# Performance work log

Measured on AMD Instinct MI355X. Metric: run time of the kernel, lower is better.

The kernel has to match this reference:

```python
import jax, jax.numpy as jnp
import numpy as np

NUM_HEADS = 16
HIDDEN = 1024
B, S = 2, 2048


def setup_inputs() -> dict:
    key = jax.random.key(0)
    ks = jax.random.split(key, 14)
    D = HIDDEN
    scale = 1.0 / np.sqrt(D)
    inp = {
        "query": jax.random.normal(ks[0], (B, S, D), jnp.float32),
        "key_in": jax.random.normal(ks[1], (B, S, D), jnp.float32),
        "value": jax.random.normal(ks[2], (B, S, D), jnp.float32),
        "group_prob": jax.random.uniform(ks[3], (B, S, S), jnp.float32),
        "mask": jax.random.randint(ks[4], (B, S, S), 0, 2, jnp.int32),
        "wq_k": jax.random.normal(ks[5], (D, D), jnp.float32) * scale,
        "wq_b": jnp.zeros((D,), jnp.float32),
        "wk_k": jax.random.normal(ks[6], (D, D), jnp.float32) * scale,
        "wk_b": jnp.zeros((D,), jnp.float32),
        "wv_k": jax.random.normal(ks[7], (D, D), jnp.float32) * scale,
        "wv_b": jnp.zeros((D,), jnp.float32),
        "wo_k": jax.random.normal(ks[8], (D, D), jnp.float32) * scale,
        "wo_b": jnp.zeros((D,), jnp.float32),
    }
    return inp


def _split_heads(x, H):
    b, s, d = x.shape
    return x.reshape(b, s, H, d // H).transpose(0, 2, 1, 3)  # (B,H,S,dh)


def reference(query, key_in, value, group_prob, mask,
              wq_k, wq_b, wk_k, wk_b, wv_k, wv_b, wo_k, wo_b):
    H = NUM_HEADS
    dh = query.shape[-1] // H
    q = _split_heads(query @ wq_k + wq_b, H)
    k = _split_heads(key_in @ wk_k + wk_b, H)
    v = _split_heads(value @ wv_k + wv_b, H)
    # scaled dot-product logits (B,H,Sq,Sk)
    logits = jnp.einsum('bhqd,bhkd->bhqk', q, k) / jnp.sqrt(jnp.asarray(dh, q.dtype))
    neg = (1.0 - mask.astype(q.dtype)) * -1e9
    logits = logits + neg[:, None, :, :]
    attn = jax.nn.softmax(logits, axis=-1)
    # Tree Transformer modulation: post-softmax elementwise scale by group_prob
    attn = attn * group_prob[:, None, :, :]
    out = jnp.einsum('bhqk,bhkd->bhqd', attn, v)
    out = out.transpose(0, 2, 1, 3).reshape(query.shape[0], -1, H * dh)
    return out @ wo_k + wo_b
```

## Files before the change

kernel.cpp:

```cpp
#include <hip/hip_runtime.h>
#include <hip/hip_bf16.h>
#include <stdint.h>

#define B_ 2
#define S_ 2048
#define D_ 1024
#define H_ 16
#define DH 64

typedef __attribute__((ext_vector_type(4))) float f32x4;
typedef __attribute__((ext_vector_type(8))) short s16x8;
typedef __attribute__((ext_vector_type(4))) short s16x4;

__device__ inline short f2bf(float f) {
  union { float f; unsigned u; } v; v.f = f;
  unsigned r = (v.u + 0x7fffu + ((v.u >> 16) & 1u)) >> 16;
  return (short)r;
}

__device__ inline float bfbits_lo(unsigned u) {
  union { unsigned x; float f; } v; v.x = u << 16; return v.f;
}
__device__ inline float bfbits_hi(unsigned u) {
  union { unsigned x; float f; } v; v.x = u & 0xffff0000u; return v.f;
}

__device__ inline float exp2v(float x) {
  float r; asm("v_exp_f32 %0, %1" : "=v"(r) : "v"(x)); return r;
}
__device__ inline unsigned cvtpk(float a, float b) {
  unsigned r; asm("v_cvt_pk_bf16_f32 %0, %1, %2" : "=v"(r) : "v"(a), "v"(b));
  return r;
}

__global__ __launch_bounds__(256) void cvt3_f32_bf16(const float* __restrict__ a,
                                                     const float* __restrict__ b,
                                                     const float* __restrict__ c,
                                                     short* oa, short* ob, short* oc,
                                                     int n) {
  int z = blockIdx.y;
  const float* in = z == 0 ? a : (z == 1 ? b : c);
  short* out = z == 0 ? oa : (z == 1 ? ob : oc);
  int i = (blockIdx.x * 256 + threadIdx.x) * 4;
  if (i < n) {
    float4 v = *(const float4*)(in + i);
    s16x4 o;
    o.x = f2bf(v.x); o.y = f2bf(v.y); o.z = f2bf(v.z); o.w = f2bf(v.w);
    *(s16x4*)(out + i) = o;
  }
}

__global__ __launch_bounds__(256) void fuse_mgp(const int* __restrict__ mask,
                                                const float* __restrict__ gp,
                                                short* __restrict__ mgp, int n) {
  int i = (blockIdx.x * 256 + threadIdx.x) * 4;
  if (i < n) {
    int4 m = *(const int4*)(mask + i);
    float4 g = *(const float4*)(gp + i);
    short b0 = f2bf(g.x); if (!b0) b0 = (short)0x0080;
    short b1 = f2bf(g.y); if (!b1) b1 = (short)0x0080;
    short b2 = f2bf(g.z); if (!b2) b2 = (short)0x0080;
    short b3 = f2bf(g.w); if (!b3) b3 = (short)0x0080;
    s16x4 o;
    o.x = m.x ? b0 : 0;
    o.y = m.y ? b1 : 0;
    o.z = m.z ? b2 : 0;
    o.w = m.w ? b3 : 0;
    *(s16x4*)(mgp + i) = o;
  }
}

__global__ __launch_bounds__(256) void transpose_cvt4(
    const float* __restrict__ i0, const float* __restrict__ i1,
    const float* __restrict__ i2, const float* __restrict__ i3,
    short* o0, short* o1, short* o2, short* o3) {
  int z = blockIdx.z;
  const float* in = z == 0 ? i0 : (z == 1 ? i1 : (z == 2 ? i2 : i3));
  short* out = z == 0 ? o0 : (z == 1 ? o1 : (z == 2 ? o2 : o3));
  __shared__ float tile[32][33];
  int bx = blockIdx.x, by = blockIdx.y;
  int x = bx * 32 + threadIdx.x;
#pragma unroll
  for (int i = 0; i < 32; i += 8) {
    int y = by * 32 + threadIdx.y + i;
    tile[threadIdx.y + i][threadIdx.x] = in[(size_t)y * D_ + x];
  }
  __syncthreads();
  int ox = by * 32 + threadIdx.x;
#pragma unroll
  for (int i = 0; i < 32; i += 8) {
    int oy = bx * 32 + threadIdx.y + i;
    out[(size_t)oy * D_ + ox] = f2bf(tile[threadIdx.x][threadIdx.y + i]);
  }
}

__global__ __launch_bounds__(256) void transpose_v(const short* __restrict__ vp,
                                                   short* __restrict__ vt) {
  __shared__ __align__(16) short t[64 * 72];
  int tid = threadIdx.x;
  int bh = blockIdx.y, b = bh >> 4, h = bh & 15;
  int s0 = blockIdx.x * 64;
  int r = tid >> 2, cc = tid & 3;
  const short* src = vp + ((size_t)(b * S_ + s0 + r)) * D_ + h * DH + cc * 16;
  s16x8 a = *(const s16x8*)src;
  s16x8 bb = *(const s16x8*)(src + 8);
  int pc = (cc ^ (r >> 4)) * 16;
  *(s16x8*)&t[r * 72 + pc] = a;
  *(s16x8*)&t[r * 72 + pc + 8] = bb;
  __syncthreads();
  int d = tid >> 2, sc = (tid & 3) * 16;
  s16x8 o0, o1;
#pragma unroll
  for (int j = 0; j < 8; ++j) {
    int row = sc + j;
    o0[j] = t[row * 72 + ((d >> 4) ^ (row >> 4)) * 16 + (d & 15)];
    int row2 = sc + 8 + j;
    o1[j] = t[row2 * 72 + ((d >> 4) ^ (row2 >> 4)) * 16 + (d & 15)];
  }
  short* dst = vt + ((size_t)(b * H_ + h) * DH + d) * S_ + s0 + sc;
  *(s16x8*)dst = o0;
  *(s16x8*)(dst + 8) = o1;
}

__device__ inline void gload_lds16(const void* g, void* l) {
  __builtin_amdgcn_global_load_lds(
      (const __attribute__((address_space(1))) unsigned*)g,
      (__attribute__((address_space(3))) unsigned*)l, 16, 0, 0);
}

#define BM 128
#define BN 128
#define BK 32

__global__ __launch_bounds__(256) void gemm_bt3(
    const short* __restrict__ A0, const short* __restrict__ A1, const short* __restrict__ A2,
    const short* __restrict__ Bt0, const short* __restrict__ Bt1, const short* __restrict__ Bt2,
    const float* __restrict__ bs0, const float* __restrict__ bs1, const float* __restrict__ bs2,
    void* C0, void* C1, void* C2,
    int M, int N, int K, int f32out, float os0, float os1, float os2) {
  int z = blockIdx.y;
  const short* A = z == 0 ? A0 : (z == 1 ? A1 : A2);
  const short* Bt = z == 0 ? Bt0 : (z == 1 ? Bt1 : Bt2);
  const float* bias = z == 0 ? bs0 : (z == 1 ? bs1 : bs2);
  void* C = z == 0 ? C0 : (z == 1 ? C1 : C2);
  float oscale = z == 0 ? os0 : (z == 1 ? os1 : os2);

  __shared__ __align__(16) short As[BM * BK];
  __shared__ __align__(16) short Bs[BN * BK];
  int tid = threadIdx.x;
  int lane = tid & 63, wave = tid >> 6;
  int l15 = lane & 15, l4 = lane >> 4;
  int ntn = N / BN;
  int bm = blockIdx.x / ntn, bn = blockIdx.x % ntn;
  int row0 = bm * BM, col0 = bn * BN;
  int wm = (wave >> 1) * 64, wn = (wave & 1) * 64;

  f32x4 acc[4][4] = {};

  for (int k0 = 0; k0 < K; k0 += BK) {
    __syncthreads();
#pragma unroll
    for (int it = 0; it < 2; ++it) {
      int ch = it * 256 + tid;
      int r = ch >> 2, c = (ch & 3) * 8;
      int ldsbase = (it * 256 + wave * 64) * 8;
      gload_lds16(A + (size_t)(row0 + r) * K + k0 + c, &As[ldsbase]);
      gload_lds16(Bt + (size_t)(col0 + r) * K + k0 + c, &Bs[ldsbase]);
    }
    __syncthreads();
    s16x8 af[4], bf[4];
#pragma unroll
    for (int mf = 0; mf < 4; ++mf)
      af[mf] = *(const s16x8*)&As[(wm + mf * 16 + l15) * BK + l4 * 8];
#pragma unroll
    for (int nf = 0; nf < 4; ++nf)
      bf[nf] = *(const s16x8*)&Bs[(wn + nf * 16 + l15) * BK + l4 * 8];
#pragma unroll
    for (int mf = 0; mf < 4; ++mf)
#pragma unroll
      for (int nf = 0; nf < 4; ++nf)
        acc[mf][nf] = __builtin_amdgcn_mfma_f32_16x16x32_bf16(af[mf], bf[nf],
                                                              acc[mf][nf], 0, 0, 0);
  }

#pragma unroll
  for (int nf = 0; nf < 4; ++nf) {
    int gcol = col0 + wn + nf * 16 + l15;
    float bv = bias[gcol];
#pragma unroll
    for (int mf = 0; mf < 4; ++mf) {
#pragma unroll
      for (int r = 0; r < 4; ++r) {
        int grow = row0 + wm + mf * 16 + l4 * 4 + r;
        float v = (acc[mf][nf][r] + bv) * oscale;
        if (f32out)
          ((float*)C)[(size_t)grow * N + gcol] = v;
        else
          ((short*)C)[(size_t)grow * N + gcol] = f2bf(v);
      }
    }
  }
}

#define QB 64
#define NB 64
#define NTILES (S_ / NB)
#define M0_SHIFT 12.0f

__global__ __launch_bounds__(256) void attn_fused(const short* __restrict__ Qp,
                                                  const short* __restrict__ Kp,
                                                  const short* __restrict__ VT,
                                                  const short* __restrict__ MGP,
                                                  short* __restrict__ ctx) {
  __shared__ __align__(16) short Ks[2][64 * 64];
  __shared__ __align__(16) short Ms[2][64 * 64];
  __shared__ __align__(16) short Vs[2][64 * 64];

  int tid = threadIdx.x, lane = tid & 63, wave = tid >> 6;
  int l15 = lane & 15, l4 = lane >> 4;
  int q0 = blockIdx.x * QB;
  int bh = blockIdx.y;
  int b = bh >> 4, h = bh & 15;
  int wq = wave * 16;

  const short* Qbase = Qp + (size_t)b * S_ * D_ + (size_t)h * DH;
  const short* Kbase = Kp + (size_t)b * S_ * D_ + (size_t)h * DH;
  const short* Vbase = VT + (size_t)(b * H_ + h) * DH * S_;
  const short* Mbase = MGP + (size_t)b * S_ * S_ + (size_t)q0 * S_;

  int i0 = tid, i1 = 256 + tid;
  int r0 = i0 >> 3, c0 = (i0 & 7) ^ (r0 & 7);
  int r1 = i1 >> 3, c1 = (i1 & 7) ^ (r1 & 7);
  int ldsA = wave * 512;
  int ldsB = 2048 + wave * 512;

#define STAGE(kv0, buf)                                                    \
  do {                                                                     \
    gload_lds16(Kbase + (size_t)((kv0) + r0) * D_ + c0 * 8, &Ks[buf][ldsA]); \
    gload_lds16(Kbase + (size_t)((kv0) + r1) * D_ + c1 * 8, &Ks[buf][ldsB]); \
    gload_lds16(Mbase + (size_t)r0 * S_ + (kv0) + c0 * 8, &Ms[buf][ldsA]);   \
    gload_lds16(Mbase + (size_t)r1 * S_ + (kv0) + c1 * 8, &Ms[buf][ldsB]);   \
    gload_lds16(Vbase + (size_t)r0 * S_ + (kv0) + c0 * 8, &Vs[buf][ldsA]);   \
    gload_lds16(Vbase + (size_t)r1 * S_ + (kv0) + c1 * 8, &Vs[buf][ldsB]);   \
  } while (0)

  s16x8 qf[2];
#pragma unroll
  for (int ks = 0; ks < 2; ++ks)
    qf[ks] = *(const s16x8*)(Qbase + (size_t)(q0 + wq + l15) * D_ + ks * 32 + l4 * 8);

  float lsum = 0.f;
  f32x4 oacc[4] = {};

  STAGE(0, 0);

  int ql = wq + l15;
  int rowoff = ql * 64;
  int q7 = l15 & 7;
  int q7l = q7 << 1;

  for (int t = 0; t < NTILES; ++t) {
    int buf = t & 1;

    if (t + 1 < NTILES) {
      STAGE((t + 1) * NB, buf ^ 1);
      asm volatile("s_waitcnt vmcnt(6)" ::: "memory");
    } else {
      asm volatile("s_waitcnt vmcnt(0)" ::: "memory");
    }
    __builtin_amdgcn_s_barrier();
    __builtin_amdgcn_sched_barrier(0);

    f32x4 sacc[4] = {};
#pragma unroll
    for (int nf = 0; nf < 4; ++nf) {
      int R = nf * 16 + l15;
#pragma unroll
      for (int ks = 0; ks < 2; ++ks) {
        s16x8 kf = *(const s16x8*)&Ks[buf][R * 64 + (((ks * 4 + l4) ^ q7) * 8)];
        sacc[nf] = __builtin_amdgcn_mfma_f32_16x16x32_bf16(kf, qf[ks], sacc[nf], 0, 0, 0);
      }
    }

#pragma unroll
    for (int nf = 0; nf < 4; ++nf) {
      int sl = ((nf * 4 + l4) ^ q7l) * 4;
      uint2 g2 = *(const uint2*)&Ms[buf][rowoff + sl];
      float gv0 = bfbits_lo(g2.x), gv1 = bfbits_hi(g2.x);
      float gv2 = bfbits_lo(g2.y), gv3 = bfbits_hi(g2.y);
      float e0 = exp2v(sacc[nf][0] - M0_SHIFT);
      float e1 = exp2v(sacc[nf][1] - M0_SHIFT);
      float e2 = exp2v(sacc[nf][2] - M0_SHIFT);
      float e3 = exp2v(sacc[nf][3] - M0_SHIFT);
      lsum += (gv0 != 0.f) ? e0 : 0.f;
      lsum += (gv1 != 0.f) ? e1 : 0.f;
      lsum += (gv2 != 0.f) ? e2 : 0.f;
      lsum += (gv3 != 0.f) ? e3 : 0.f;
      uint2 wp;
      wp.x = cvtpk(e0 * gv0, e1 * gv1);
      wp.y = cvtpk(e2 * gv2, e3 * gv3);
      *(uint2*)&Ms[buf][rowoff + sl] = wp;
    }

#pragma unroll
    for (int ks = 0; ks < 2; ++ks) {
      s16x8 pa = *(const s16x8*)&Ms[buf][rowoff + (((ks * 4 + l4) ^ q7) * 8)];
#pragma unroll
      for (int df = 0; df < 4; ++df) {
        s16x8 vf = *(const s16x8*)&Vs[buf][(df * 16 + l15) * 64 +
                                           (((ks * 4 + l4) ^ q7) * 8)];
        oacc[df] = __builtin_amdgcn_mfma_f32_16x16x32_bf16(vf, pa, oacc[df], 0, 0, 0);
      }
    }

    asm volatile("s_waitcnt lgkmcnt(0)" ::: "memory");
    __builtin_amdgcn_s_barrier();
  }
#undef STAGE

  lsum += __shfl_xor(lsum, 16);
  lsum += __shfl_xor(lsum, 32);
  float inv = 1.f / lsum;
  short* crow = ctx + ((size_t)(b * S_ + q0 + wq + l15)) * D_ + h * DH;
#pragma unroll
  for (int df = 0; df < 4; ++df) {
    uint2 o;
    o.x = cvtpk(oacc[df][0] * inv, oacc[df][1] * inv);
    o.y = cvtpk(oacc[df][2] * inv, oacc[df][3] * inv);
    *(uint2*)(crow + df * 16 + l4 * 4) = o;
  }
}

extern "C" void kernel_launch(void* const* d_in, const int* in_sizes, int n_in,
                              void* d_out, int out_size, void* d_ws, size_t ws_size,
                              hipStream_t stream) {
  const float* query = (const float*)d_in[0];
  const float* key_in = (const float*)d_in[1];
  const float* value = (const float*)d_in[2];
  const float* group_prob = (const float*)d_in[3];
  const int* mask = (const int*)d_in[4];
  const float* wq_k = (const float*)d_in[5];
  const float* wq_b = (const float*)d_in[6];
  const float* wk_k = (const float*)d_in[7];
  const float* wk_b = (const float*)d_in[8];
  const float* wv_k = (const float*)d_in[9];
  const float* wv_b = (const float*)d_in[10];
  const float* wo_k = (const float*)d_in[11];
  const float* wo_b = (const float*)d_in[12];
  float* out = (float*)d_out;

  short* ws = (short*)d_ws;
  const size_t NT = (size_t)B_ * S_ * D_;
  short* qbf = ws;
  short* kbf = qbf + NT;
  short* vbf = kbf + NT;
  short* wqt = vbf + NT;
  short* wkt = wqt + (size_t)D_ * D_;
  short* wvt = wkt + (size_t)D_ * D_;
  short* wot = wvt + (size_t)D_ * D_;
  short* qp = wot + (size_t)D_ * D_;
  short* kp = qp + NT;
  short* vp = kp + NT;
  short* ctx = vp + NT;
  short* mgp = ws;
  short* vt = vbf;

  int nblk = (int)(NT / 4 / 256);
  cvt3_f32_bf16<<<dim3(nblk, 3), 256, 0, stream>>>(query, key_in, value,
                                                   qbf, kbf, vbf, (int)NT);

  dim3 tb(32, 8);
  transpose_cvt4<<<dim3(D_ / 32, D_ / 32, 4), tb, 0, stream>>>(
      wq_k, wk_k, wv_k, wo_k, wqt, wkt, wvt, wot);

  int M = B_ * S_;
  int gblocks = (M / BM) * (D_ / BN);
  const float QSCALE = 0.125f * 1.4426950408889634f;
  gemm_bt3<<<dim3(gblocks, 3), 256, 0, stream>>>(
      qbf, kbf, vbf, wqt, wkt, wvt, wq_b, wk_b, wv_b, qp, kp, vp,
      M, D_, D_, 0, QSCALE, 1.0f, 1.0f);

  int nmg = B_ * S_ * S_;
  fuse_mgp<<<nmg / 4 / 256, 256, 0, stream>>>(mask, group_prob, mgp, nmg);
  transpose_v<<<dim3(S_ / 64, B_ * H_), 256, 0, stream>>>(vp, vt);

  dim3 ag(S_ / QB, B_ * H_);
  attn_fused<<<ag, 256, 0, stream>>>(qp, kp, vt, mgp, ctx);

  gemm_bt3<<<dim3(gblocks, 1), 256, 0, stream>>>(
      ctx, ctx, ctx, wot, wot, wot, wo_b, wo_b, wo_b, out, out, out,
      M, D_, D_, 1, 1.0f, 1.0f, 1.0f);
}
```

Measured before the change: 192.6 us.

## Double attention query tile per block and deepen GEMM K tile

The attention kernel now handles 128 query rows per block, with each wave computing two 16-row fragments. Every staged K/V tile is therefore reused across twice as many queries, which halves K/V global traffic, and the mask/group-prob staging grows to four loads per thread. The projection GEMM moves from BK=32 to BK=64, doing two MFMA k-steps per barrier pair to cut synchronisation overhead. The cost is more registers and LDS per block, and the attention grid has half as many blocks, which may reduce occupancy.

Result: no change. 195.2 us (+1.3%).

```diff
diff --git a/kernel.cpp b/kernel.cpp
--- a/kernel.cpp
+++ b/kernel.cpp
@@ -130,7 +130,7 @@
 
 #define BM 128
 #define BN 128
-#define BK 32
+#define BK 64
 
 __global__ __launch_bounds__(256) void gemm_bt3(
     const short* __restrict__ A0, const short* __restrict__ A1, const short* __restrict__ A2,
@@ -160,27 +160,30 @@
   for (int k0 = 0; k0 < K; k0 += BK) {
     __syncthreads();
 #pragma unroll
-    for (int it = 0; it < 2; ++it) {
+    for (int it = 0; it < 4; ++it) {
       int ch = it * 256 + tid;
-      int r = ch >> 2, c = (ch & 3) * 8;
+      int r = ch >> 3, c = (ch & 7) * 8;
       int ldsbase = (it * 256 + wave * 64) * 8;
       gload_lds16(A + (size_t)(row0 + r) * K + k0 + c, &As[ldsbase]);
       gload_lds16(Bt + (size_t)(col0 + r) * K + k0 + c, &Bs[ldsbase]);
     }
     __syncthreads();
-    s16x8 af[4], bf[4];
-#pragma unroll
-    for (int mf = 0; mf < 4; ++mf)
-      af[mf] = *(const s16x8*)&As[(wm + mf * 16 + l15) * BK + l4 * 8];
-#pragma unroll
-    for (int nf = 0; nf < 4; ++nf)
-      bf[nf] = *(const s16x8*)&Bs[(wn + nf * 16 + l15) * BK + l4 * 8];
-#pragma unroll
-    for (int mf = 0; mf < 4; ++mf)
+#pragma unroll
+    for (int ks = 0; ks < 2; ++ks) {
+      s16x8 af[4], bf[4];
+#pragma unroll
+      for (int mf = 0; mf < 4; ++mf)
+        af[mf] = *(const s16x8*)&As[(wm + mf * 16 + l15) * BK + ks * 32 + l4 * 8];
 #pragma unroll
       for (int nf = 0; nf < 4; ++nf)
-        acc[mf][nf] = __builtin_amdgcn_mfma_f32_16x16x32_bf16(af[mf], bf[nf],
-                                                              acc[mf][nf], 0, 0, 0);
+        bf[nf] = *(const s16x8*)&Bs[(wn + nf * 16 + l15) * BK + ks * 32 + l4 * 8];
+#pragma unroll
+      for (int mf = 0; mf < 4; ++mf)
+#pragma unroll
+        for (int nf = 0; nf < 4; ++nf)
+          acc[mf][nf] = __builtin_amdgcn_mfma_f32_16x16x32_bf16(af[mf], bf[nf],
+                                                                acc[mf][nf], 0, 0, 0);
+    }
   }
 
 #pragma unroll
@@ -202,7 +205,7 @@
   }
 }
 
-#define QB 64
+#define QB 128
 #define NB 64
 #define NTILES (S_ / NB)
 #define M0_SHIFT 12.0f
@@ -213,7 +216,7 @@
                                                   const short* __restrict__ MGP,
                                                   short* __restrict__ ctx) {
   __shared__ __align__(16) short Ks[2][64 * 64];
-  __shared__ __align__(16) short Ms[2][64 * 64];
+  __shared__ __align__(16) short Ms[2][QB * 64];
   __shared__ __align__(16) short Vs[2][64 * 64];
 
   int tid = threadIdx.x, lane = tid & 63, wave = tid >> 6;
@@ -221,7 +224,7 @@
   int q0 = blockIdx.x * QB;
   int bh = blockIdx.y;
   int b = bh >> 4, h = bh & 15;
-  int wq = wave * 16;
+  int wq = wave * 32;
 
   const short* Qbase = Qp + (size_t)b * S_ * D_ + (size_t)h * DH;
   const short* Kbase = Kp + (size_t)b * S_ * D_ + (size_t)h * DH;
@@ -233,83 +236,107 @@
   int r1 = i1 >> 3, c1 = (i1 & 7) ^ (r1 & 7);
   int ldsA = wave * 512;
   int ldsB = 2048 + wave * 512;
-
-#define STAGE(kv0, buf)                                                    \
-  do {                                                                     \
-    gload_lds16(Kbase + (size_t)((kv0) + r0) * D_ + c0 * 8, &Ks[buf][ldsA]); \
-    gload_lds16(Kbase + (size_t)((kv0) + r1) * D_ + c1 * 8, &Ks[buf][ldsB]); \
-    gload_lds16(Mbase + (size_t)r0 * S_ + (kv0) + c0 * 8, &Ms[buf][ldsA]);   \
-    gload_lds16(Mbase + (size_t)r1 * S_ + (kv0) + c1 * 8, &Ms[buf][ldsB]);   \
-    gload_lds16(Vbase + (size_t)r0 * S_ + (kv0) + c0 * 8, &Vs[buf][ldsA]);   \
-    gload_lds16(Vbase + (size_t)r1 * S_ + (kv0) + c1 * 8, &Vs[buf][ldsB]);   \
+  int mr[4], mc[4], mlds[4];
+#pragma unroll
+  for (int it = 0; it < 4; ++it) {
+    int ch = it * 256 + tid;
+    mr[it] = ch >> 3;
+    mc[it] = (ch & 7) ^ (mr[it] & 7);
+    mlds[it] = (it * 256 + wave * 64) * 8;
+  }
+
+#define STAGE(kv0, buf)                                                       \
+  do {                                                                        \
+    gload_lds16(Kbase + (size_t)((kv0) + r0) * D_ + c0 * 8, &Ks[buf][ldsA]);  \
+    gload_lds16(Kbase + (size_t)((kv0) + r1) * D_ + c1 * 8, &Ks[buf][ldsB]);  \
+    gload_lds16(Vbase + (size_t)r0 * S_ + (kv0) + c0 * 8, &Vs[buf][ldsA]);    \
+    gload_lds16(Vbase + (size_t)r1 * S_ + (kv0) + c1 * 8, &Vs[buf][ldsB]);    \
+    gload_lds16(Mbase + (size_t)mr[0] * S_ + (kv0) + mc[0] * 8, &Ms[buf][mlds[0]]); \
+    gload_lds16(Mbase + (size_t)mr[1] * S_ + (kv0) + mc[1] * 8, &Ms[buf][mlds[1]]); \
+    gload_lds16(Mbase + (size_t)mr[2] * S_ + (kv0) + mc[2] * 8, &Ms[buf][mlds[2]]); \
+    gload_lds16(Mbase + (size_t)mr[3] * S_ + (kv0) + mc[3] * 8, &Ms[buf][mlds[3]]); \
   } while (0)
 
-  s16x8 qf[2];
-#pragma unroll
-  for (int ks = 0; ks < 2; ++ks)
-    qf[ks] = *(const s16x8*)(Qbase + (size_t)(q0 + wq + l15) * D_ + ks * 32 + l4 * 8);
-
-  float lsum = 0.f;
-  f32x4 oacc[4] = {};
+  s16x8 qf[2][2];
+#pragma unroll
+  for (int mf = 0; mf < 2; ++mf)
+#pragma unroll
+    for (int ks = 0; ks < 2; ++ks)
+      qf[mf][ks] = *(const s16x8*)(Qbase + (size_t)(q0 + wq + mf * 16 + l15) * D_ +
+                                   ks * 32 + l4 * 8);
+
+  float lsum[2] = {0.f, 0.f};
+  f32x4 oacc[2][4] = {};
 
   STAGE(0, 0);
 
-  int ql = wq + l15;
-  int rowoff = ql * 64;
   int q7 = l15 & 7;
   int q7l = q7 << 1;
+  int rowoff[2] = {(wq + l15) * 64, (wq + 16 + l15) * 64};
 
   for (int t = 0; t < NTILES; ++t) {
     int buf = t & 1;
 
     if (t + 1 < NTILES) {
       STAGE((t + 1) * NB, buf ^ 1);
-      asm volatile("s_waitcnt vmcnt(6)" ::: "memory");
+      asm volatile("s_waitcnt vmcnt(8)" ::: "memory");
     } else {
       asm volatile("s_waitcnt vmcnt(0)" ::: "memory");
     }
     __builtin_amdgcn_s_barrier();
     __builtin_amdgcn_sched_barrier(0);
 
-    f32x4 sacc[4] = {};
+    f32x4 sacc[2][4] = {};
 #pragma unroll
     for (int nf = 0; nf < 4; ++nf) {
       int R = nf * 16 + l15;
 #pragma unroll
       for (int ks = 0; ks < 2; ++ks) {
         s16x8 kf = *(const s16x8*)&Ks[buf][R * 64 + (((ks * 4 + l4) ^ q7) * 8)];
-        sacc[nf] = __builtin_amdgcn_mfma_f32_16x16x32_bf16(kf, qf[ks], sacc[nf], 0, 0, 0);
+#pragma unroll
+        for (int mf = 0; mf < 2; ++mf)
+          sacc[mf][nf] = __builtin_amdgcn_mfma_f32_16x16x32_bf16(kf, qf[mf][ks],
+                                                                 sacc[mf][nf], 0, 0, 0);
       }
     }
 
 #pragma unroll
-    for (int nf = 0; nf < 4; ++nf) {
-      int sl = ((nf * 4 + l4) ^ q7l) * 4;
-      uint2 g2 = *(const uint2*)&Ms[buf][rowoff + sl];
-      float gv0 = bfbits_lo(g2.x), gv1 = bfbits_hi(g2.x);
-      float gv2 = bfbits_lo(g2.y), gv3 = bfbits_hi(g2.y);
-      float e0 = exp2v(sacc[nf][0] - M0_SHIFT);
-      float e1 = exp2v(sacc[nf][1] - M0_SHIFT);
-      float e2 = exp2v(sacc[nf][2] - M0_SHIFT);
-      float e3 = exp2v(sacc[nf][3] - M0_SHIFT);
-      lsum += (gv0 != 0.f) ? e0 : 0.f;
-      lsum += (gv1 != 0.f) ? e1 : 0.f;
-      lsum += (gv2 != 0.f) ? e2 : 0.f;
-      lsum += (gv3 != 0.f) ? e3 : 0.f;
-      uint2 wp;
-      wp.x = cvtpk(e0 * gv0, e1 * gv1);
-      wp.y = cvtpk(e2 * gv2, e3 * gv3);
-      *(uint2*)&Ms[buf][rowoff + sl] = wp;
+    for (int mf = 0; mf < 2; ++mf) {
+#pragma unroll
+      for (int nf = 0; nf < 4; ++nf) {
+        int sl = ((nf * 4 + l4) ^ q7l) * 4;
+        uint2 g2 = *(const uint2*)&Ms[buf][rowoff[mf] + sl];
+        float gv0 = bfbits_lo(g2.x), gv1 = bfbits_hi(g2.x);
+        float gv2 = bfbits_lo(g2.y), gv3 = bfbits_hi(g2.y);
+        float e0 = exp2v(sacc[mf][nf][0] - M0_SHIFT);
+        float e1 = exp2v(sacc[mf][nf][1] - M0_SHIFT);
+        float e2 = exp2v(sacc[mf][nf][2] - M0_SHIFT);
+        float e3 = exp2v(sacc[mf][nf][3] - M0_SHIFT);
+        lsum[mf] += (gv0 != 0.f) ? e0 : 0.f;
+        lsum[mf] += (gv1 != 0.f) ? e1 : 0.f;
+        lsum[mf] += (gv2 != 0.f) ? e2 : 0.f;
+        lsum[mf] += (gv3 != 0.f) ? e3 : 0.f;
+        uint2 wp;
+        wp.x = cvtpk(e0 * gv0, e1 * gv1);
+        wp.y = cvtpk(e2 * gv2, e3 * gv3);
+        *(uint2*)&Ms[buf][rowoff[mf] + sl] = wp;
+      }
     }
 
 #pragma unroll
     for (int ks = 0; ks < 2; ++ks) {
-      s16x8 pa = *(const s16x8*)&Ms[buf][rowoff + (((ks * 4 + l4) ^ q7) * 8)];
+      s16x8 pa[2];
+#pragma unroll
+      for (int mf = 0; mf < 2; ++mf)
+        pa[mf] = *(const s16x8*)&Ms[buf][rowoff[mf] + (((ks * 4 + l4) ^ q7) * 8)];
 #pragma unroll
       for (int df = 0; df < 4; ++df) {
         s16x8 vf = *(const s16x8*)&Vs[buf][(df * 16 + l15) * 64 +
                                            (((ks * 4 + l4) ^ q7) * 8)];
-        oacc[df] = __builtin_amdgcn_mfma_f32_16x16x32_bf16(vf, pa, oacc[df], 0, 0, 0);
+#pragma unroll
+        for (int mf = 0; mf < 2; ++mf)
+          oacc[mf][df] = __builtin_amdgcn_mfma_f32_16x16x32_bf16(vf, pa[mf],
+                                                                 oacc[mf][df], 0, 0, 0);
       }
     }
 
@@ -318,16 +345,20 @@
   }
 #undef STAGE
 
-  lsum += __shfl_xor(lsum, 16);
-  lsum += __shfl_xor(lsum, 32);
-  float inv = 1.f / lsum;
-  short* crow = ctx + ((size_t)(b * S_ + q0 + wq + l15)) * D_ + h * DH;
-#pragma unroll
-  for (int df = 0; df < 4; ++df) {
-    uint2 o;
-    o.x = cvtpk(oacc[df][0] * inv, oacc[df][1] * inv);
-    o.y = cvtpk(oacc[df][2] * inv, oacc[df][3] * inv);
-    *(uint2*)(crow + df * 16 + l4 * 4) = o;
+#pragma unroll
+  for (int mf = 0; mf < 2; ++mf) {
+    float ls = lsum[mf];
+    ls += __shfl_xor(ls, 16);
+    ls += __shfl_xor(ls, 32);
+    float inv = 1.f / ls;
+    short* crow = ctx + ((size_t)(b * S_ + q0 + wq + mf * 16 + l15)) * D_ + h * DH;
+#pragma unroll
+    for (int df = 0; df < 4; ++df) {
+      uint2 o;
+      o.x = cvtpk(oacc[mf][df][0] * inv, oacc[mf][df][1] * inv);
+      o.y = cvtpk(oacc[mf][df][2] * inv, oacc[mf][df][3] * inv);
+      *(uint2*)(crow + df * 16 + l4 * 4) = o;
+    }
   }
 }
 
```
